# Performance work log

Measured on AMD Instinct MI355X. Metric: run time of the kernel, lower is better.

The kernel has to match this reference:

```python
import jax, jax.numpy as jnp
import numpy as np

N_NODES = 100000
N_EDGES = 1600000
N_GRAPHS = 512
IN_F = 16
HID = 64
NEG_SLOPE = 0.2


def gat_conv(x, edge_src, edge_dst, W, att_src, att_dst, bias):
    """PyG GATConv, heads=1, concat=True, add_self_loops handled by caller."""
    h = x @ W                                  # [N, HID]
    a_src = h @ att_src                        # [N]
    a_dst = h @ att_dst                        # [N]
    logits = jax.nn.leaky_relu(a_src[edge_src] + a_dst[edge_dst], NEG_SLOPE)  # [E]
    # segment softmax over destination nodes
    m = jax.ops.segment_max(logits, edge_dst, num_segments=N_NODES)
    m = jnp.where(jnp.isfinite(m), m, 0.0)
    e = jnp.exp(logits - m[edge_dst])
    denom = jax.ops.segment_sum(e, edge_dst, num_segments=N_NODES)
    alpha = e / (denom[edge_dst] + 1e-16)      # [E]
    out = jax.ops.segment_sum(h[edge_src] * alpha[:, None], edge_dst,
                              num_segments=N_NODES)
    return out + bias


def setup_inputs() -> dict:
    key = jax.random.key(0)
    ks = jax.random.split(key, 12)
    inp = {
        "x": jax.random.normal(ks[0], (N_NODES, IN_F), jnp.float32),
        "edge_index": jax.random.randint(ks[1], (2, N_EDGES), 0, N_NODES, jnp.int64),
        "batch": jnp.sort(jax.random.randint(ks[2], (N_NODES,), 0, N_GRAPHS, jnp.int64)),
        # conv1 params
        "W1": jax.random.normal(ks[3], (IN_F, HID), jnp.float32) * (1.0 / np.sqrt(IN_F)),
        "att_src1": jax.random.normal(ks[4], (HID,), jnp.float32) * 0.1,
        "att_dst1": jax.random.normal(ks[5], (HID,), jnp.float32) * 0.1,
        "b1": jnp.zeros((HID,), jnp.float32),
        # conv2 params
        "W2": jax.random.normal(ks[6], (HID, HID), jnp.float32) * (1.0 / np.sqrt(HID)),
        "att_src2": jax.random.normal(ks[7], (HID,), jnp.float32) * 0.1,
        "att_dst2": jax.random.normal(ks[8], (HID,), jnp.float32) * 0.1,
        "b2": jnp.zeros((HID,), jnp.float32),
        # final linear
        "fc_w": jax.random.normal(ks[9], (2 * HID, 1), jnp.float32) * (1.0 / np.sqrt(2 * HID)),
        "fc_b": jnp.zeros((1,), jnp.float32),
    }
    return inp


def reference(x, edge_index, batch, W1, att_src1, att_dst1, b1,
              W2, att_src2, att_dst2, b2, fc_w, fc_b):
    # add self loops once (PyG GATConv add_self_loops=True)
    loop = jnp.arange(N_NODES, dtype=edge_index.dtype)
    src = jnp.concatenate([edge_index[0], loop])
    dst = jnp.concatenate([edge_index[1], loop])

    h = jax.nn.relu(x)
    h = gat_conv(h, src, dst, W1, att_src1, att_dst1, b1)
    h = jax.nn.relu(h)
    h = gat_conv(h, src, dst, W2, att_src2, att_dst2, b2)
    h = jax.nn.relu(h)

    # global max + mean pool over graphs
    gmax = jax.ops.segment_max(h, batch, num_segments=N_GRAPHS)
    cnt = jax.ops.segment_sum(jnp.ones((N_NODES,), h.dtype), batch,
                              num_segments=N_GRAPHS)
    gsum = jax.ops.segment_sum(h, batch, num_segments=N_GRAPHS)
    nonempty = cnt[:, None] > 0
    gmax = jnp.where(nonempty, gmax, 0.0)
    gmean = gsum / jnp.maximum(cnt[:, None], 1.0)
    pooled = jnp.concatenate([gmax, gmean], axis=1)   # [G, 2*HID]
    return pooled @ fc_w + fc_b
```

## Files before the change

kernel.cpp:

```cpp
#include <hip/hip_runtime.h>
#include <hip/hip_fp16.h>

static constexpr int NN   = 100000;
static constexpr int NE   = 1600000;
static constexpr int ET   = NE + NN;
static constexpr int NG   = 512;
static constexpr int INF_ = 16;
static constexpr int HID  = 64;
static constexpr int BKT_SH = 7;
static constexpr int NBKT = (NN + 127) / 128;
static constexpr int NCH  = 256;
static constexpr int CHUNK = (ET + NCH - 1) / NCH;
static constexpr int M_   = NBKT * NCH;
static constexpr int SBLK = (M_ + 1023) / 1024;
#define NEG_SLOPE 0.2f

typedef _Float16 f16x8 __attribute__((ext_vector_type(8)));
typedef float    f32x4 __attribute__((ext_vector_type(4)));

__device__ __forceinline__ float lrelu(float x) { return x > 0.f ? x : NEG_SLOPE * x; }

__global__ __launch_bounds__(256) void k_node1(
    const float* __restrict__ x, const float* __restrict__ W,
    const float* __restrict__ atts, const float* __restrict__ attd,
    __half* __restrict__ h, float* __restrict__ a_s, float* __restrict__ a_d)
{
  const int wv = threadIdx.x >> 6, ln = threadIdx.x & 63;
  const int lr = ln & 15, lk = ln >> 4;
  f16x8 Bh[4], Bl[4];
#pragma unroll
  for (int ct = 0; ct < 4; ++ct) {
    f16x8 bh = {}, bl = {};
    if (lk < 2) {
#pragma unroll
      for (int j = 0; j < 8; ++j) {
        float w = W[(lk * 8 + j) * HID + ct * 16 + lr];
        _Float16 hh = (_Float16)w;
        bh[j] = hh; bl[j] = (_Float16)(w - (float)hh);
      }
    }
    Bh[ct] = bh; Bl[ct] = bl;
  }
  const int NT = NN / 16;
  for (int nt = blockIdx.x * 4 + wv; nt < NT; nt += gridDim.x * 4) {
    const int nbase = nt * 16;
    f16x8 Ah = {}, Al = {};
    if (lk < 2) {
      const float* xr = x + (size_t)(nbase + lr) * INF_ + lk * 8;
#pragma unroll
      for (int j = 0; j < 8; ++j) {
        float v = xr[j]; v = v > 0.f ? v : 0.f;
        _Float16 hh = (_Float16)v;
        Ah[j] = hh; Al[j] = (_Float16)(v - (float)hh);
      }
    }
    f32x4 C[4];
#pragma unroll
    for (int ct = 0; ct < 4; ++ct) {
      f32x4 c = {0.f, 0.f, 0.f, 0.f};
      c = __builtin_amdgcn_mfma_f32_16x16x32_f16(Ah, Bh[ct], c, 0, 0, 0);
      c = __builtin_amdgcn_mfma_f32_16x16x32_f16(Ah, Bl[ct], c, 0, 0, 0);
      c = __builtin_amdgcn_mfma_f32_16x16x32_f16(Al, Bh[ct], c, 0, 0, 0);
      C[ct] = c;
    }
    float asp[4] = {0.f, 0.f, 0.f, 0.f}, adp[4] = {0.f, 0.f, 0.f, 0.f};
#pragma unroll
    for (int ct = 0; ct < 4; ++ct) {
      float at_s = atts[ct * 16 + lr], at_d = attd[ct * 16 + lr];
#pragma unroll
      for (int r = 0; r < 4; ++r) {
        float v = C[ct][r];
        h[(size_t)(nbase + lk * 4 + r) * HID + ct * 16 + lr] = __float2half(v);
        asp[r] += v * at_s; adp[r] += v * at_d;
      }
    }
#pragma unroll
    for (int o = 1; o < 16; o <<= 1) {
#pragma unroll
      for (int r = 0; r < 4; ++r) {
        asp[r] += __shfl_xor(asp[r], o);
        adp[r] += __shfl_xor(adp[r], o);
      }
    }
    if (lr == 0) {
#pragma unroll
      for (int r = 0; r < 4; ++r) {
        a_s[nbase + lk * 4 + r] = asp[r];
        a_d[nbase + lk * 4 + r] = adp[r];
      }
    }
  }
}

__global__ __launch_bounds__(256) void k_node2(
    const float* __restrict__ act, const float* __restrict__ W,
    const float* __restrict__ atts, const float* __restrict__ attd,
    __half* __restrict__ h, float* __restrict__ a_s, float* __restrict__ a_d)
{
  const int wv = threadIdx.x >> 6, ln = threadIdx.x & 63;
  const int lr = ln & 15, lk = ln >> 4;
  f16x8 Bh[4][2], Bl[4][2];
#pragma unroll
  for (int ct = 0; ct < 4; ++ct)
#pragma unroll
    for (int ks = 0; ks < 2; ++ks) {
      f16x8 bh, bl;
#pragma unroll
      for (int j = 0; j < 8; ++j) {
        float w = W[(ks * 32 + lk * 8 + j) * HID + ct * 16 + lr];
        _Float16 hh = (_Float16)w;
        bh[j] = hh; bl[j] = (_Float16)(w - (float)hh);
      }
      Bh[ct][ks] = bh; Bl[ct][ks] = bl;
    }
  const int NT = NN / 16;
  for (int nt = blockIdx.x * 4 + wv; nt < NT; nt += gridDim.x * 4) {
    const int nbase = nt * 16;
    const float* ar = act + (size_t)(nbase + lr) * HID + lk * 8;
    f16x8 A0h, A0l, A1h, A1l;
#pragma unroll
    for (int j = 0; j < 8; ++j) {
      float v = ar[j];
      _Float16 hh = (_Float16)v;
      A0h[j] = hh; A0l[j] = (_Float16)(v - (float)hh);
    }
#pragma unroll
    for (int j = 0; j < 8; ++j) {
      float v = ar[32 + j];
      _Float16 hh = (_Float16)v;
      A1h[j] = hh; A1l[j] = (_Float16)(v - (float)hh);
    }
    f32x4 C[4];
#pragma unroll
    for (int ct = 0; ct < 4; ++ct) {
      f32x4 c = {0.f, 0.f, 0.f, 0.f};
      c = __builtin_amdgcn_mfma_f32_16x16x32_f16(A0h, Bh[ct][0], c, 0, 0, 0);
      c = __builtin_amdgcn_mfma_f32_16x16x32_f16(A0h, Bl[ct][0], c, 0, 0, 0);
      c = __builtin_amdgcn_mfma_f32_16x16x32_f16(A0l, Bh[ct][0], c, 0, 0, 0);
      c = __builtin_amdgcn_mfma_f32_16x16x32_f16(A1h, Bh[ct][1], c, 0, 0, 0);
      c = __builtin_amdgcn_mfma_f32_16x16x32_f16(A1h, Bl[ct][1], c, 0, 0, 0);
      c = __builtin_amdgcn_mfma_f32_16x16x32_f16(A1l, Bh[ct][1], c, 0, 0, 0);
      C[ct] = c;
    }
    float asp[4] = {0.f, 0.f, 0.f, 0.f}, adp[4] = {0.f, 0.f, 0.f, 0.f};
#pragma unroll
    for (int ct = 0; ct < 4; ++ct) {
      float at_s = atts[ct * 16 + lr], at_d = attd[ct * 16 + lr];
#pragma unroll
      for (int r = 0; r < 4; ++r) {
        float v = C[ct][r];
        h[(size_t)(nbase + lk * 4 + r) * HID + ct * 16 + lr] = __float2half(v);
        asp[r] += v * at_s; adp[r] += v * at_d;
      }
    }
#pragma unroll
    for (int o = 1; o < 16; o <<= 1) {
#pragma unroll
      for (int r = 0; r < 4; ++r) {
        asp[r] += __shfl_xor(asp[r], o);
        adp[r] += __shfl_xor(adp[r], o);
      }
    }
    if (lr == 0) {
#pragma unroll
      for (int r = 0; r < 4; ++r) {
        a_s[nbase + lk * 4 + r] = asp[r];
        a_d[nbase + lk * 4 + r] = adp[r];
      }
    }
  }
}

__global__ __launch_bounds__(256) void k_cnt(const int* __restrict__ ei,
                                             unsigned* __restrict__ counts)
{
  __shared__ unsigned lc[NBKT];
  for (int i = threadIdx.x; i < NBKT; i += 256) lc[i] = 0;
  __syncthreads();
  const int b = blockIdx.x;
  const int beg = b * CHUNK, end = min(ET, beg + CHUNK);
  for (int e = beg + threadIdx.x; e < end; e += 256) {
    int d = (e < NE) ? ei[NE + e] : e - NE;
    atomicAdd(&lc[d >> BKT_SH], 1u);
  }
  __syncthreads();
  for (int k = threadIdx.x; k < NBKT; k += 256) counts[k * NCH + b] = lc[k];
}

__global__ __launch_bounds__(256) void k_scan1(const unsigned* __restrict__ counts,
                                               unsigned* __restrict__ bsums)
{
  __shared__ unsigned red[4];
  const int t = threadIdx.x;
  const int base = blockIdx.x * 1024 + t * 4;
  unsigned s = 0;
#pragma unroll
  for (int k = 0; k < 4; ++k) { int i = base + k; if (i < M_) s += counts[i]; }
#pragma unroll
  for (int o = 32; o > 0; o >>= 1) s += __shfl_xor(s, o);
  if ((t & 63) == 0) red[t >> 6] = s;
  __syncthreads();
  if (t == 0) bsums[blockIdx.x] = red[0] + red[1] + red[2] + red[3];
}

__global__ __launch_bounds__(64) void k_scan2(unsigned* __restrict__ bsums)
{
  const int ln = threadIdx.x;
  unsigned carry = 0;
  for (int base = 0; base < SBLK; base += 64) {
    int i = base + ln;
    unsigned orig = (i < SBLK) ? bsums[i] : 0;
    unsigned v = orig;
#pragma unroll
    for (int o = 1; o < 64; o <<= 1) { unsigned tv = __shfl_up(v, o); if (ln >= o) v += tv; }
    if (i < SBLK) bsums[i] = carry + v - orig;
    carry += __shfl(v, 63);
  }
}

__global__ __launch_bounds__(256) void k_scan3(unsigned* __restrict__ counts,
                                               const unsigned* __restrict__ bsums)
{
  __shared__ unsigned wsum[4];
  const int t = threadIdx.x;
  const int base = blockIdx.x * 1024 + t * 4;
  unsigned d[4]; unsigned s = 0;
#pragma unroll
  for (int k = 0; k < 4; ++k) { int i = base + k; d[k] = (i < M_) ? counts[i] : 0; s += d[k]; }
  unsigned v = s;
#pragma unroll
  for (int o = 1; o < 64; o <<= 1) { unsigned tv = __shfl_up(v, o); if ((t & 63) >= o) v += tv; }
  if ((t & 63) == 63) wsum[t >> 6] = v;
  __syncthreads();
  unsigned woff = 0;
  for (int w = 0; w < (t >> 6); ++w) woff += wsum[w];
  unsigned excl = woff + (v - s) + bsums[blockIdx.x];
#pragma unroll
  for (int k = 0; k < 4; ++k) {
    int i = base + k;
    if (i < M_) counts[i] = excl;
    excl += d[k];
  }
}

__global__ __launch_bounds__(256) void k_place(const int* __restrict__ ei,
                                               const unsigned* __restrict__ S,
                                               int2* __restrict__ pairs)
{
  __shared__ unsigned cur[NBKT];
  const int b = blockIdx.x;
  for (int k = threadIdx.x; k < NBKT; k += 256) cur[k] = S[k * NCH + b];
  __syncthreads();
  const int beg = b * CHUNK, end = min(ET, beg + CHUNK);
  for (int e = beg + threadIdx.x; e < end; e += 256) {
    int s, d;
    if (e < NE) { s = ei[e]; d = ei[NE + e]; } else { s = d = e - NE; }
    unsigned pos = atomicAdd(&cur[d >> BKT_SH], 1u);
    pairs[pos] = make_int2(s, d);
  }
}

__global__ __launch_bounds__(256) void k_bcsr(const int2* __restrict__ pairs,
                                              const unsigned* __restrict__ S,
                                              unsigned* __restrict__ rowptr,
                                              unsigned* __restrict__ deg,
                                              int* __restrict__ es)
{
  __shared__ unsigned cnt[128], cur[128], wtot[2];
  const int b = blockIdx.x, t = threadIdx.x;
  const unsigned base = S[b * NCH];
  const unsigned m = ((b + 1 < NBKT) ? S[(b + 1) * NCH] : (unsigned)ET) - base;
  if (t < 128) cnt[t] = 0;
  __syncthreads();
  for (unsigned j = t; j < m; j += 256)
    atomicAdd(&cnt[pairs[base + j].y & 127], 1u);
  __syncthreads();
  unsigned c = 0, v = 0;
  if (t < 128) {
    c = cnt[t]; v = c;
    const int ln = t & 63;
#pragma unroll
    for (int o = 1; o < 64; o <<= 1) { unsigned tv = __shfl_up(v, o); if (ln >= o) v += tv; }
    if (ln == 63) wtot[t >> 6] = v;
  }
  __syncthreads();
  if (t < 128) {
    unsigned excl = v - c + ((t >= 64) ? wtot[0] : 0);
    cur[t] = excl;
    int node = (b << BKT_SH) + t;
    if (node < NN) { rowptr[node] = base + excl; deg[node] = c; }
  }
  __syncthreads();
  for (unsigned j = t; j < m; j += 256) {
    int2 p = pairs[base + j];
    unsigned pos = atomicAdd(&cur[p.y & 127], 1u);
    es[base + pos] = p.x;
  }
}

__global__ __launch_bounds__(256) void k_attn(
    const int* __restrict__ es, const unsigned* __restrict__ rowptr,
    const unsigned* __restrict__ deg, const float* __restrict__ a_s,
    const float* __restrict__ a_d, float* __restrict__ alpha)
{
  const int wv = threadIdx.x >> 6, ln = threadIdx.x & 63;
  const int n = blockIdx.x * 4 + wv;
  const unsigned beg = rowptr[n], dg = deg[n];
  const float ad = a_d[n];
  const unsigned j0 = beg + (unsigned)ln;
  float l0 = -1e30f, m = -1e30f;
  if ((unsigned)ln < dg) { l0 = lrelu(a_s[es[j0]] + ad); m = l0; }
  for (unsigned j = beg + 64 + ln; j < beg + dg; j += 64)
    m = fmaxf(m, lrelu(a_s[es[j]] + ad));
#pragma unroll
  for (int o = 32; o > 0; o >>= 1) m = fmaxf(m, __shfl_xor(m, o));
  float ev0 = ((unsigned)ln < dg) ? __expf(l0 - m) : 0.f;
  float den = ev0;
  for (unsigned j = beg + 64 + ln; j < beg + dg; j += 64)
    den += __expf(lrelu(a_s[es[j]] + ad) - m);
#pragma unroll
  for (int o = 32; o > 0; o >>= 1) den += __shfl_xor(den, o);
  const float inv = 1.f / (den + 1e-16f);
  if ((unsigned)ln < dg) alpha[j0] = ev0 * inv;
  for (unsigned j = beg + 64 + ln; j < beg + dg; j += 64)
    alpha[j] = __expf(lrelu(a_s[es[j]] + ad) - m) * inv;
}

__global__ __launch_bounds__(256) void k_wsum(
    const int* __restrict__ es, const float* __restrict__ alpha,
    const unsigned* __restrict__ rowptr, const unsigned* __restrict__ deg,
    const __half* __restrict__ h, const float* __restrict__ bias,
    float* __restrict__ act)
{
  const int wv = threadIdx.x >> 6, ln = threadIdx.x & 63;
  const int n = blockIdx.x * 4 + wv;
  const unsigned beg  = (unsigned)__builtin_amdgcn_readfirstlane((int)rowptr[n]);
  const unsigned dg   = (unsigned)__builtin_amdgcn_readfirstlane((int)deg[n]);
  const unsigned end  = beg + dg;
  const unsigned last = end - 1;
  float acc = 0.f;
  for (unsigned j = beg; j < end; j += 16) {
    int s[16]; float al[16]; __half hv[16];
#pragma unroll
    for (int k = 0; k < 16; ++k) {
      unsigned jj = j + (unsigned)k;
      unsigned jc = jj < last ? jj : last;
      s[k]  = es[jc];
      al[k] = (jj < end) ? alpha[jc] : 0.f;
    }
#pragma unroll
    for (int k = 0; k < 16; ++k) hv[k] = h[(size_t)s[k] * HID + ln];
#pragma unroll
    for (int k = 0; k < 16; ++k) acc += al[k] * __half2float(hv[k]);
  }
  float v = acc + bias[ln];
  act[(size_t)n * HID + ln] = v > 0.f ? v : 0.f;
}

__global__ __launch_bounds__(256) void k_pool(
    const float* __restrict__ act, const int* __restrict__ batch,
    unsigned* __restrict__ gmax, float* __restrict__ gsum, unsigned* __restrict__ cnt)
{
  const int wv = threadIdx.x >> 6, ln = threadIdx.x & 63;
  const int base = (blockIdx.x * 4 + wv) * 64;
  if (base >= NN) return;
  const int end = min(NN, base + 64);
  float rmax = 0.f, rsum = 0.f;
  int cg = batch[base], run = 0;
  for (int n = base; n < end; ++n) {
    int g = batch[n];
    if (g != cg) {
      atomicMax(&gmax[cg * HID + ln], __float_as_uint(rmax));
      unsafeAtomicAdd(&gsum[cg * HID + ln], rsum);
      if (ln == 0) atomicAdd(&cnt[cg], (unsigned)run);
      rmax = 0.f; rsum = 0.f; run = 0; cg = g;
    }
    float v = act[n * HID + ln];
    rmax = fmaxf(rmax, v); rsum += v; ++run;
  }
  atomicMax(&gmax[cg * HID + ln], __float_as_uint(rmax));
  unsafeAtomicAdd(&gsum[cg * HID + ln], rsum);
  if (ln == 0) atomicAdd(&cnt[cg], (unsigned)run);
}

__global__ __launch_bounds__(256) void k_final(
    const unsigned* __restrict__ gmax, const float* __restrict__ gsum,
    const unsigned* __restrict__ cnt, const float* __restrict__ fcw,
    const float* __restrict__ fcb, float* __restrict__ out)
{
  const int wv = threadIdx.x >> 6, ln = threadIdx.x & 63;
  const int g = blockIdx.x * 4 + wv;
  if (g >= NG) return;
  float c = (float)cnt[g];
  float mx = __uint_as_float(gmax[g * HID + ln]);
  float mean = gsum[g * HID + ln] / fmaxf(c, 1.f);
  float v = mx * fcw[ln] + mean * fcw[HID + ln];
#pragma unroll
  for (int o = 32; o > 0; o >>= 1) v += __shfl_xor(v, o);
  if (ln == 0) out[g] = v + fcb[0];
}

extern "C" void kernel_launch(void* const* d_in, const int* in_sizes, int n_in,
                              void* d_out, int out_size, void* d_ws, size_t ws_size,
                              hipStream_t stream)
{
  const float* x    = (const float*)d_in[0];
  const int*   ei   = (const int*)d_in[1];
  const int*   batch= (const int*)d_in[2];
  const float* W1   = (const float*)d_in[3];
  const float* as1  = (const float*)d_in[4];
  const float* ad1  = (const float*)d_in[5];
  const float* b1   = (const float*)d_in[6];
  const float* W2   = (const float*)d_in[7];
  const float* as2  = (const float*)d_in[8];
  const float* ad2  = (const float*)d_in[9];
  const float* b2   = (const float*)d_in[10];
  const float* fcw  = (const float*)d_in[11];
  const float* fcb  = (const float*)d_in[12];
  float* out = (float*)d_out;

  __half* h       = (__half*)d_ws;
  float* act      = (float*)(h + (size_t)NN * HID);
  float* a_s      = act + (size_t)NN * HID;
  float* a_d      = a_s + NN;
  unsigned* deg   = (unsigned*)(a_d + NN);
  unsigned* rowptr= deg + NN;
  unsigned* counts= rowptr + NN;
  unsigned* bsums = counts + 200704;
  int* es         = (int*)(bsums + 256);
  float* alpha    = (float*)(es + ET);
  unsigned* gmax  = (unsigned*)(alpha + ET);
  float* gsum     = (float*)(gmax + NG * HID);
  unsigned* cnt   = (unsigned*)(gsum + NG * HID);
  int2* pairs     = (int2*)act;

  k_cnt  <<<NCH, 256, 0, stream>>>(ei, counts);
  k_scan1<<<SBLK, 256, 0, stream>>>(counts, bsums);
  k_scan2<<<1, 64, 0, stream>>>(bsums);
  k_scan3<<<SBLK, 256, 0, stream>>>(counts, bsums);
  k_place<<<NCH, 256, 0, stream>>>(ei, counts, pairs);
  k_bcsr <<<NBKT, 256, 0, stream>>>(pairs, counts, rowptr, deg, es);

  k_node1<<<512, 256, 0, stream>>>(x, W1, as1, ad1, h, a_s, a_d);
  k_attn <<<NN / 4, 256, 0, stream>>>(es, rowptr, deg, a_s, a_d, alpha);
  k_wsum <<<NN / 4, 256, 0, stream>>>(es, alpha, rowptr, deg, h, b1, act);

  k_node2<<<512, 256, 0, stream>>>(act, W2, as2, ad2, h, a_s, a_d);
  k_attn <<<NN / 4, 256, 0, stream>>>(es, rowptr, deg, a_s, a_d, alpha);
  k_wsum <<<NN / 4, 256, 0, stream>>>(es, alpha, rowptr, deg, h, b2, act);

  hipMemsetAsync(gmax, 0, sizeof(unsigned) * NG * HID, stream);
  hipMemsetAsync(gsum, 0, sizeof(float) * NG * HID, stream);
  hipMemsetAsync(cnt,  0, sizeof(unsigned) * NG, stream);
  k_pool<<<(NN + 255) / 256, 256, 0, stream>>>(act, batch, gmax, gsum, cnt);
  k_final<<<NG / 4, 256, 0, stream>>>(gmax, gsum, cnt, fcw, fcb, out);
}
```

Measured before the change: 267.3 us.

## Fuse attention softmax and weighted aggregation into one GAT kernel

Merges the per-node attention kernel and the weighted-sum kernel into a single kernel. Each wave first computes the row max over its edges, then in one pass computes the exponentials, accumulates the denominator and the weighted feature sum, and normalizes at the end. This drops the alpha buffer write and read plus one launch per layer. In exchange every lane redundantly gathers a_s and recomputes the logits, and the max pass is run lane-uniformly instead of spread across lanes.

```diff
diff --git a/kernel.cpp b/kernel.cpp
--- a/kernel.cpp
+++ b/kernel.cpp
@@ -298,39 +298,11 @@
   }
 }
 
-__global__ __launch_bounds__(256) void k_attn(
+__global__ __launch_bounds__(256) void k_gat(
     const int* __restrict__ es, const unsigned* __restrict__ rowptr,
     const unsigned* __restrict__ deg, const float* __restrict__ a_s,
-    const float* __restrict__ a_d, float* __restrict__ alpha)
-{
-  const int wv = threadIdx.x >> 6, ln = threadIdx.x & 63;
-  const int n = blockIdx.x * 4 + wv;
-  const unsigned beg = rowptr[n], dg = deg[n];
-  const float ad = a_d[n];
-  const unsigned j0 = beg + (unsigned)ln;
-  float l0 = -1e30f, m = -1e30f;
-  if ((unsigned)ln < dg) { l0 = lrelu(a_s[es[j0]] + ad); m = l0; }
-  for (unsigned j = beg + 64 + ln; j < beg + dg; j += 64)
-    m = fmaxf(m, lrelu(a_s[es[j]] + ad));
-#pragma unroll
-  for (int o = 32; o > 0; o >>= 1) m = fmaxf(m, __shfl_xor(m, o));
-  float ev0 = ((unsigned)ln < dg) ? __expf(l0 - m) : 0.f;
-  float den = ev0;
-  for (unsigned j = beg + 64 + ln; j < beg + dg; j += 64)
-    den += __expf(lrelu(a_s[es[j]] + ad) - m);
-#pragma unroll
-  for (int o = 32; o > 0; o >>= 1) den += __shfl_xor(den, o);
-  const float inv = 1.f / (den + 1e-16f);
-  if ((unsigned)ln < dg) alpha[j0] = ev0 * inv;
-  for (unsigned j = beg + 64 + ln; j < beg + dg; j += 64)
-    alpha[j] = __expf(lrelu(a_s[es[j]] + ad) - m) * inv;
-}
-
-__global__ __launch_bounds__(256) void k_wsum(
-    const int* __restrict__ es, const float* __restrict__ alpha,
-    const unsigned* __restrict__ rowptr, const unsigned* __restrict__ deg,
-    const __half* __restrict__ h, const float* __restrict__ bias,
-    float* __restrict__ act)
+    const float* __restrict__ a_d, const __half* __restrict__ h,
+    const float* __restrict__ bias, float* __restrict__ act)
 {
   const int wv = threadIdx.x >> 6, ln = threadIdx.x & 63;
   const int n = blockIdx.x * 4 + wv;
@@ -338,22 +310,40 @@
   const unsigned dg   = (unsigned)__builtin_amdgcn_readfirstlane((int)deg[n]);
   const unsigned end  = beg + dg;
   const unsigned last = end - 1;
-  float acc = 0.f;
+  const float ad = a_d[n];
+  float m = -1e30f;
   for (unsigned j = beg; j < end; j += 16) {
-    int s[16]; float al[16]; __half hv[16];
+    float l[16];
 #pragma unroll
     for (int k = 0; k < 16; ++k) {
       unsigned jj = j + (unsigned)k;
       unsigned jc = jj < last ? jj : last;
-      s[k]  = es[jc];
-      al[k] = (jj < end) ? alpha[jc] : 0.f;
+      float lv = lrelu(a_s[es[jc]] + ad);
+      l[k] = (jj < end) ? lv : -1e30f;
+    }
+#pragma unroll
+    for (int k = 0; k < 16; ++k) m = fmaxf(m, l[k]);
+  }
+  float acc = 0.f, den = 0.f;
+  for (unsigned j = beg; j < end; j += 16) {
+    int s[16]; float ev[16]; __half hv[16];
+#pragma unroll
+    for (int k = 0; k < 16; ++k) {
+      unsigned jj = j + (unsigned)k;
+      unsigned jc = jj < last ? jj : last;
+      s[k] = es[jc];
+      float lv = lrelu(a_s[s[k]] + ad);
+      ev[k] = (jj < end) ? __expf(lv - m) : 0.f;
     }
 #pragma unroll
     for (int k = 0; k < 16; ++k) hv[k] = h[(size_t)s[k] * HID + ln];
 #pragma unroll
-    for (int k = 0; k < 16; ++k) acc += al[k] * __half2float(hv[k]);
-  }
-  float v = acc + bias[ln];
+    for (int k = 0; k < 16; ++k) {
+      den += ev[k];
+      acc += ev[k] * __half2float(hv[k]);
+    }
+  }
+  float v = acc / (den + 1e-16f) + bias[ln];
   act[(size_t)n * HID + ln] = v > 0.f ? v : 0.f;
 }
 
@@ -428,8 +418,7 @@
   unsigned* counts= rowptr + NN;
   unsigned* bsums = counts + 200704;
   int* es         = (int*)(bsums + 256);
-  float* alpha    = (float*)(es + ET);
-  unsigned* gmax  = (unsigned*)(alpha + ET);
+  unsigned* gmax  = (unsigned*)(es + ET);
   float* gsum     = (float*)(gmax + NG * HID);
   unsigned* cnt   = (unsigned*)(gsum + NG * HID);
   int2* pairs     = (int2*)act;
@@ -442,12 +431,10 @@
   k_bcsr <<<NBKT, 256, 0, stream>>>(pairs, counts, rowptr, deg, es);
 
   k_node1<<<512, 256, 0, stream>>>(x, W1, as1, ad1, h, a_s, a_d);
-  k_attn <<<NN / 4, 256, 0, stream>>>(es, rowptr, deg, a_s, a_d, alpha);
-  k_wsum <<<NN / 4, 256, 0, stream>>>(es, alpha, rowptr, deg, h, b1, act);
+  k_gat  <<<NN / 4, 256, 0, stream>>>(es, rowptr, deg, a_s, a_d, h, b1, act);
 
   k_node2<<<512, 256, 0, stream>>>(act, W2, as2, ad2, h, a_s, a_d);
-  k_attn <<<NN / 4, 256, 0, stream>>>(es, rowptr, deg, a_s, a_d, alpha);
-  k_wsum <<<NN / 4, 256, 0, stream>>>(es, alpha, rowptr, deg, h, b2, act);
+  k_gat  <<<NN / 4, 256, 0, stream>>>(es, rowptr, deg, a_s, a_d, h, b2, act);
 
   hipMemsetAsync(gmax, 0, sizeof(unsigned) * NG * HID, stream);
   hipMemsetAsync(gsum, 0, sizeof(float) * NG * HID, stream);
```

New measurement: 429.8 us. 1.61x slower.
